# Kernel tuning notes

Hardware: AMD Instinct MI355X
Metric: run time of the kernel (lower is better)

Reference implementation:

```python
import jax, jax.numpy as jnp
import numpy as np

DIM = 2048
NUM_HEADS = 16
HEAD_DIM = DIM // NUM_HEADS
SCALE = 1.0 / float(np.sqrt(HEAD_DIM))


def setup_inputs() -> dict:
    key = jax.random.key(0)
    ks = jax.random.split(key, 7)
    B, L = 2, 2048
    x = jax.random.normal(ks[0], (B, L, DIM), dtype=jnp.float32)
    s = 1.0 / np.sqrt(DIM)
    # nn.Linear stores weight as [out, in]; y = x @ W.T + b
    Wq = jax.random.uniform(ks[1], (DIM, DIM), jnp.float32, -s, s)
    bq = jax.random.uniform(ks[2], (DIM,), jnp.float32, -s, s)
    Wk = jax.random.uniform(ks[3], (DIM, DIM), jnp.float32, -s, s)
    bk = jax.random.uniform(ks[4], (DIM,), jnp.float32, -s, s)
    Wv = jax.random.uniform(ks[5], (DIM, DIM), jnp.float32, -s, s)
    bv = jax.random.uniform(ks[6], (DIM,), jnp.float32, -s, s)
    return {"x": x, "Wq": Wq, "bq": bq, "Wk": Wk, "bk": bk, "Wv": Wv, "bv": bv}


def _attn(x, Wq, bq, Wk, bk, Wv, bv):
    B, L, D = x.shape
    H, Hd = NUM_HEADS, HEAD_DIM
    # projections: x @ W.T + b, then split heads -> [B, H, L, Hd]
    q = (x @ Wq.T + bq).reshape(B, L, H, Hd).transpose(0, 2, 1, 3)
    k = (x @ Wk.T + bk).reshape(B, L, H, Hd).transpose(0, 2, 1, 3)
    v = (x @ Wv.T + bv).reshape(B, L, H, Hd).transpose(0, 2, 1, 3)
    scores = jnp.einsum("bhqd,bhkd->bhqk", q, k) * SCALE  # [B,H,L,L]
    attn = jax.nn.softmax(scores, axis=-1)
    out = jnp.einsum("bhqk,bhkd->bhqd", attn, v)
    return out.transpose(0, 2, 1, 3).reshape(B, L, D)


def reference(x, Wq, bq, Wk, bk, Wv, bv):
    return _attn(x, Wq, bq, Wk, bk, Wv, bv)
```

## Files before the change

### kernel.cpp

```cpp
#include <hip/hip_runtime.h>
#include <stdint.h>

typedef unsigned short u16;
typedef __attribute__((ext_vector_type(8))) short short8;
typedef __attribute__((ext_vector_type(16))) float f32x16;

#define ATTN_SCALE 0.08838834764831845f

__device__ __forceinline__ u16 f2bf(float f) {
  union { float f; uint32_t u; } a; a.f = f;
  return (u16)((a.u + 0x7fffu + ((a.u >> 16) & 1u)) >> 16);
}

__device__ __forceinline__ void async16(const u16* g, u16* lds) {
  __builtin_amdgcn_global_load_lds(
      (const __attribute__((address_space(1))) void*)g,
      (__attribute__((address_space(3))) void*)lds, 16, 0, 0);
}

__global__ void cvt_kernel(const float* __restrict__ src, u16* __restrict__ dst, int n8) {
  int i = blockIdx.x * 256 + threadIdx.x;
  if (i >= n8) return;
  const float4* s4 = (const float4*)src;
  float4 a = s4[2 * i], c = s4[2 * i + 1];
  union { u16 h[8]; uint4 v; } o;
  o.h[0] = f2bf(a.x); o.h[1] = f2bf(a.y); o.h[2] = f2bf(a.z); o.h[3] = f2bf(a.w);
  o.h[4] = f2bf(c.x); o.h[5] = f2bf(c.y); o.h[6] = f2bf(c.z); o.h[7] = f2bf(c.w);
  ((uint4*)dst)[i] = o.v;
}

__global__ void cvtw_kernel(const float* __restrict__ w0, const float* __restrict__ w1,
                            const float* __restrict__ w2, u16* __restrict__ dst) {
  int z = blockIdx.y;
  const float* src = (z == 0) ? w0 : (z == 1) ? w1 : w2;
  int i = blockIdx.x * 256 + threadIdx.x;
  const float4* s4 = (const float4*)src;
  float4 a = s4[2 * i], c = s4[2 * i + 1];
  union { u16 h[8]; uint4 v; } o;
  o.h[0] = f2bf(a.x); o.h[1] = f2bf(a.y); o.h[2] = f2bf(a.z); o.h[3] = f2bf(a.w);
  o.h[4] = f2bf(c.x); o.h[5] = f2bf(c.y); o.h[6] = f2bf(c.z); o.h[7] = f2bf(c.w);
  ((uint4*)(dst + (size_t)z * 4194304))[i] = o.v;
}

__global__ __launch_bounds__(256, 4) void qkv_gemm(
    const u16* __restrict__ xb, const u16* __restrict__ Wb,
    const float* __restrict__ bq, const float* __restrict__ bk, const float* __restrict__ bv,
    u16* __restrict__ qkv) {
  __shared__ __align__(16) u16 As[2][128 * 32];
  __shared__ __align__(16) u16 Bs[2][128 * 32];
  const int z = blockIdx.z;
  const int n0 = blockIdx.x * 128, m0 = blockIdx.y * 128;
  const u16* Bw = Wb + (size_t)z * (2048u * 2048u);
  const float* bias = (z == 0) ? bq : (z == 1) ? bk : bv;
  u16* dst = qkv + (size_t)z * 8388608u;
  const int t = threadIdx.x, wave = t >> 6, lane = t & 63;
  const int wm = wave >> 1, wn = wave & 1, l31 = lane & 31, h = lane >> 5;

  int soff[2], goff[2];
#pragma unroll
  for (int p = 0; p < 2; ++p) {
    const int s = p * 256 + wave * 64 + lane;
    const int R = s >> 4, j = s & 15, u = j ^ (R & 15);
    const int m = R * 4 + (u >> 2), c = u & 3;
    soff[p] = s * 8;
    goff[p] = m * 2048 + c * 8;
  }
  int fr16[2][2], fR15[2][2];
  const int q4 = (l31 & 3) * 4;
#pragma unroll
  for (int i = 0; i < 2; ++i) {
    const int mA = wm * 64 + i * 32 + l31, mB = wn * 64 + i * 32 + l31;
    fr16[0][i] = (mA >> 2) * 16; fR15[0][i] = (mA >> 2) & 15;
    fr16[1][i] = (mB >> 2) * 16; fR15[1][i] = (mB >> 2) & 15;
  }

  f32x16 acc[2][2];
#pragma unroll
  for (int i = 0; i < 2; ++i)
#pragma unroll
    for (int j = 0; j < 2; ++j)
#pragma unroll
      for (int r = 0; r < 16; ++r) acc[i][j][r] = 0.f;

  const u16* Abase = xb + (size_t)m0 * 2048;
  const u16* Bbase = Bw + (size_t)n0 * 2048;

#pragma unroll 1
  for (int n = 0; n < 64; ++n) {
    if (n == 0) {
#pragma unroll
      for (int p = 0; p < 2; ++p) {
        async16(Abase + goff[p], &As[0][soff[p]]);
        async16(Bbase + goff[p], &Bs[0][soff[p]]);
      }
    }
    __syncthreads();
    const int cur = n & 1;
    if (n + 1 < 64) {
      const int k1 = (n + 1) * 32;
#pragma unroll
      for (int p = 0; p < 2; ++p) {
        async16(Abase + goff[p] + k1, &As[cur ^ 1][soff[p]]);
        async16(Bbase + goff[p] + k1, &Bs[cur ^ 1][soff[p]]);
      }
    }
#pragma unroll
    for (int ks = 0; ks < 2; ++ks) {
      const int c = ks * 2 + h;
      short8 af[2], bf[2];
#pragma unroll
      for (int i = 0; i < 2; ++i) {
        af[i] = *(const short8*)&As[cur][(fr16[0][i] + ((q4 + c) ^ fR15[0][i])) * 8];
        bf[i] = *(const short8*)&Bs[cur][(fr16[1][i] + ((q4 + c) ^ fR15[1][i])) * 8];
      }
#pragma unroll
      for (int i = 0; i < 2; ++i)
#pragma unroll
        for (int j = 0; j < 2; ++j)
          acc[i][j] = __builtin_amdgcn_mfma_f32_32x32x16_bf16(af[i], bf[j], acc[i][j], 0, 0, 0);
    }
  }

#pragma unroll
  for (int j = 0; j < 2; ++j) {
    const int col = n0 + wn * 64 + j * 32 + l31;
    const float bb_ = bias[col];
    const int hh = col >> 7, hd = col & 127;
#pragma unroll
    for (int i = 0; i < 2; ++i) {
#pragma unroll
      for (int g = 0; g < 4; ++g) {
        const int lbase = m0 + wm * 64 + i * 32 + 8 * g + 4 * h;
        const int bb = lbase >> 11, l0 = lbase & 2047;
        if (z == 2) {
          union { u16 q[4]; uint2 d; } pk;
#pragma unroll
          for (int rr = 0; rr < 4; ++rr) pk.q[rr] = f2bf(acc[i][j][4 * g + rr] + bb_);
          *(uint2*)&dst[((size_t)(bb * 16 + hh) * 128 + hd) * 2048 + l0] = pk.d;
        } else {
#pragma unroll
          for (int rr = 0; rr < 4; ++rr)
            dst[((size_t)(bb * 16 + hh) * 2048 + (l0 + rr)) * 128 + hd] =
                f2bf(acc[i][j][4 * g + rr] + bb_);
        }
      }
    }
  }
}

__global__ __launch_bounds__(256, 1) void attn_kernel(
    const u16* __restrict__ Qg,
    const u16* __restrict__ Kg,
    const u16* __restrict__ Vtg,
    float* __restrict__ out) {
  __shared__ __align__(16) u16 Ks[2][64 * 128];
  __shared__ __align__(16) u16 Vs[2][128 * 64];
  const int bh = blockIdx.y, q0 = blockIdx.x * 256;
  const int t = threadIdx.x, wave = t >> 6, lane = t & 63;
  const int l31 = lane & 31, h = lane >> 5;
  const u16* Qp = Qg + (size_t)bh * 262144;
  const u16* Kp = Kg + (size_t)bh * 262144;
  const u16* Vp = Vtg + (size_t)bh * 262144;
  const int b = bh >> 4, hd = bh & 15;

  short8 qf[2][8];
#pragma unroll
  for (int qs = 0; qs < 2; ++qs) {
    const int qrow = q0 + wave * 64 + qs * 32 + l31;
#pragma unroll
    for (int s = 0; s < 8; ++s)
      qf[qs][s] = *(const short8*)&Qp[(size_t)qrow * 128 + s * 16 + h * 8];
  }

  int kOff[4], kSlot[4], vOff[4], vSlot[4];
#pragma unroll
  for (int p = 0; p < 4; ++p) {
    const int s = p * 256 + wave * 64 + lane;
    const int rk = s >> 4, gk = (s & 15) ^ (rk & 15);
    kSlot[p] = s * 8; kOff[p] = rk * 128 + gk * 8;
    const int rv = s >> 3, gv = (s & 7) ^ (rv & 7);
    vSlot[p] = s * 8; vOff[p] = rv * 2048 + gv * 8;
  }

  f32x16 oac[2][4];
#pragma unroll
  for (int qs = 0; qs < 2; ++qs)
#pragma unroll
    for (int dt = 0; dt < 4; ++dt)
#pragma unroll
      for (int r = 0; r < 16; ++r) oac[qs][dt][r] = 0.f;
  float den[2] = {0.f, 0.f};

#pragma unroll 1
  for (int n = 0; n < 32; ++n) {
    if (n == 0) {
#pragma unroll
      for (int p = 0; p < 4; ++p) {
        async16(Kp + kOff[p], &Ks[0][kSlot[p]]);
        async16(Vp + vOff[p], &Vs[0][vSlot[p]]);
      }
    }
    __syncthreads();
    const int cur = n & 1;
    if (n + 1 < 32) {
      const int k1 = (n + 1) * 64;
#pragma unroll
      for (int p = 0; p < 4; ++p) {
        async16(Kp + (size_t)k1 * 128 + kOff[p], &Ks[cur ^ 1][kSlot[p]]);
        async16(Vp + (size_t)k1 + vOff[p], &Vs[cur ^ 1][vSlot[p]]);
      }
    }

#pragma unroll
    for (int T = 0; T < 2; ++T) {
      const int krow = T * 32 + l31;
      f32x16 sc[2];
#pragma unroll
      for (int qs = 0; qs < 2; ++qs)
#pragma unroll
        for (int r = 0; r < 16; ++r) sc[qs][r] = 0.f;
#pragma unroll
      for (int s = 0; s < 8; ++s) {
        const short8 kf = *(const short8*)&Ks[cur][(krow * 16 + ((2 * s + h) ^ (krow & 15))) * 8];
        sc[0] = __builtin_amdgcn_mfma_f32_32x32x16_bf16(kf, qf[0][s], sc[0], 0, 0, 0);
        sc[1] = __builtin_amdgcn_mfma_f32_32x32x16_bf16(kf, qf[1][s], sc[1], 0, 0, 0);
      }
      uint32_t pp[2][8], x[2][8];
#pragma unroll
      for (int qs = 0; qs < 2; ++qs) {
#pragma unroll
        for (int i = 0; i < 8; ++i) {
          const float e0 = __expf(fminf(sc[qs][2 * i] * ATTN_SCALE, 80.f));
          const float e1 = __expf(fminf(sc[qs][2 * i + 1] * ATTN_SCALE, 80.f));
          den[qs] += e0 + e1;
          union { float f; uint32_t u; } u0, u1; u0.f = e0; u1.f = e1;
          pp[qs][i] = ((u1.u + 0x8000u) & 0xffff0000u) | ((u0.u + 0x8000u) >> 16);
        }
#pragma unroll
        for (int i = 0; i < 8; ++i) x[qs][i] = __shfl_xor(pp[qs][i], 32, 64);
      }
#pragma unroll
      for (int ks = 0; ks < 2; ++ks) {
        const int o0 = ks * 4;
        union { uint32_t u[4]; short8 s8; } bfp[2];
#pragma unroll
        for (int qs = 0; qs < 2; ++qs) {
          bfp[qs].u[0] = h ? x[qs][o0 + 2] : pp[qs][o0 + 0];
          bfp[qs].u[1] = h ? x[qs][o0 + 3] : pp[qs][o0 + 1];
          bfp[qs].u[2] = h ? pp[qs][o0 + 2] : x[qs][o0 + 0];
          bfp[qs].u[3] = h ? pp[qs][o0 + 3] : x[qs][o0 + 1];
        }
        const int gk = T * 4 + ks * 2 + h;
#pragma unroll
        for (int dt = 0; dt < 4; ++dt) {
          const int vrow = dt * 32 + l31;
          const short8 vf = *(const short8*)&Vs[cur][(vrow * 8 + (gk ^ (vrow & 7))) * 8];
          oac[0][dt] = __builtin_amdgcn_mfma_f32_32x32x16_bf16(vf, bfp[0].s8, oac[0][dt], 0, 0, 0);
          oac[1][dt] = __builtin_amdgcn_mfma_f32_32x32x16_bf16(vf, bfp[1].s8, oac[1][dt], 0, 0, 0);
        }
      }
    }
  }

#pragma unroll
  for (int qs = 0; qs < 2; ++qs) {
    float d2 = den[qs] + __shfl_xor(den[qs], 32, 64);
    const float inv = 1.f / d2;
    const int qrow = q0 + wave * 64 + qs * 32 + l31;
#pragma unroll
    for (int dt = 0; dt < 4; ++dt) {
#pragma unroll
      for (int g4 = 0; g4 < 4; ++g4) {
        float4 o;
        o.x = oac[qs][dt][4 * g4 + 0] * inv;
        o.y = oac[qs][dt][4 * g4 + 1] * inv;
        o.z = oac[qs][dt][4 * g4 + 2] * inv;
        o.w = oac[qs][dt][4 * g4 + 3] * inv;
        const int d = dt * 32 + g4 * 8 + h * 4;
        *(float4*)&out[((size_t)(b * 2048 + qrow)) * 2048 + hd * 128 + d] = o;
      }
    }
  }
}

extern "C" void kernel_launch(void* const* d_in, const int* in_sizes, int n_in,
                              void* d_out, int out_size, void* d_ws, size_t ws_size,
                              hipStream_t stream) {
  const float* x  = (const float*)d_in[0];
  const float* Wq = (const float*)d_in[1];
  const float* bq = (const float*)d_in[2];
  const float* Wk = (const float*)d_in[3];
  const float* bk = (const float*)d_in[4];
  const float* Wv = (const float*)d_in[5];
  const float* bv = (const float*)d_in[6];
  float* out = (float*)d_out;
  if (ws_size < 92274688u) return;

  u16* xb  = (u16*)d_ws;
  u16* Wb  = xb + 8388608;
  u16* qkv = Wb + 12582912;

  cvt_kernel<<<4096, 256, 0, stream>>>(x, xb, 1048576);
  cvtw_kernel<<<dim3(2048, 3), 256, 0, stream>>>(Wq, Wk, Wv, Wb);
  qkv_gemm<<<dim3(16, 32, 3), 256, 0, stream>>>(xb, Wb, bq, bk, bv, qkv);
  attn_kernel<<<dim3(8, 32), 256, 0, stream>>>(qkv, qkv + 8388608, qkv + 16777216, out);
}
```

Before: 384.7 us.

## Split attention key tiles across wave pairs and reduce partial outputs in LDS

Each attention block now covers 128 queries instead of 256. Its four waves form two query groups times two key-half groups: each wave handles one 32-key sub-tile per 64-key chunk and keeps its own output accumulator. The partial outputs and denominators are combined through an LDS union that reuses the K/V buffers, and the launch bound allows two blocks per CU. The goal is to double the grid from 256 to 512 blocks so the 256 CUs are better filled and latency is hidden. The cost is halved K/V reuse per block, extra LDS reduction traffic and syncs, and more register pressure under the 2-block bound.

After: 391.2 us. Within noise of the previous version (+1.7%).

```diff
diff --git a/kernel.cpp b/kernel.cpp
--- a/kernel.cpp
+++ b/kernel.cpp
@@ -148,16 +148,19 @@
   }
 }
 
-__global__ __launch_bounds__(256, 1) void attn_kernel(
+__global__ __launch_bounds__(256, 2) void attn_kernel(
     const u16* __restrict__ Qg,
     const u16* __restrict__ Kg,
     const u16* __restrict__ Vtg,
     float* __restrict__ out) {
-  __shared__ __align__(16) u16 Ks[2][64 * 128];
-  __shared__ __align__(16) u16 Vs[2][128 * 64];
-  const int bh = blockIdx.y, q0 = blockIdx.x * 256;
+  __shared__ __align__(16) union {
+    struct { u16 Ks[2][64 * 128]; u16 Vs[2][128 * 64]; } lp;
+    struct { float dred[2][128]; float Ored[2][64][136]; } ep;
+  } sm;
+  const int bh = blockIdx.y, q0 = blockIdx.x * 128;
   const int t = threadIdx.x, wave = t >> 6, lane = t & 63;
   const int l31 = lane & 31, h = lane >> 5;
+  const int qg = wave & 1, T = wave >> 1;
   const u16* Qp = Qg + (size_t)bh * 262144;
   const u16* Kp = Kg + (size_t)bh * 262144;
   const u16* Vp = Vtg + (size_t)bh * 262144;
@@ -166,21 +169,22 @@
   short8 qf[2][8];
 #pragma unroll
   for (int qs = 0; qs < 2; ++qs) {
-    const int qrow = q0 + wave * 64 + qs * 32 + l31;
+    const int qrow = q0 + qg * 64 + qs * 32 + l31;
 #pragma unroll
     for (int s = 0; s < 8; ++s)
       qf[qs][s] = *(const short8*)&Qp[(size_t)qrow * 128 + s * 16 + h * 8];
   }
 
-  int kOff[4], kSlot[4], vOff[4], vSlot[4];
+  int kOff[4], vOff[4];
 #pragma unroll
   for (int p = 0; p < 4; ++p) {
     const int s = p * 256 + wave * 64 + lane;
     const int rk = s >> 4, gk = (s & 15) ^ (rk & 15);
-    kSlot[p] = s * 8; kOff[p] = rk * 128 + gk * 8;
+    kOff[p] = rk * 128 + gk * 8;
     const int rv = s >> 3, gv = (s & 7) ^ (rv & 7);
-    vSlot[p] = s * 8; vOff[p] = rv * 2048 + gv * 8;
-  }
+    vOff[p] = rv * 2048 + gv * 8;
+  }
+  const int slot0 = (wave * 64 + lane) * 8;
 
   f32x16 oac[2][4];
 #pragma unroll
@@ -190,14 +194,15 @@
 #pragma unroll
       for (int r = 0; r < 16; ++r) oac[qs][dt][r] = 0.f;
   float den[2] = {0.f, 0.f};
+  const int krow = T * 32 + l31;
 
 #pragma unroll 1
   for (int n = 0; n < 32; ++n) {
     if (n == 0) {
 #pragma unroll
       for (int p = 0; p < 4; ++p) {
-        async16(Kp + kOff[p], &Ks[0][kSlot[p]]);
-        async16(Vp + vOff[p], &Vs[0][vSlot[p]]);
+        async16(Kp + kOff[p], &sm.lp.Ks[0][slot0 + p * 2048]);
+        async16(Vp + vOff[p], &sm.lp.Vs[0][slot0 + p * 2048]);
       }
     }
     __syncthreads();
@@ -206,79 +211,100 @@
       const int k1 = (n + 1) * 64;
 #pragma unroll
       for (int p = 0; p < 4; ++p) {
-        async16(Kp + (size_t)k1 * 128 + kOff[p], &Ks[cur ^ 1][kSlot[p]]);
-        async16(Vp + (size_t)k1 + vOff[p], &Vs[cur ^ 1][vSlot[p]]);
-      }
-    }
-
-#pragma unroll
-    for (int T = 0; T < 2; ++T) {
-      const int krow = T * 32 + l31;
-      f32x16 sc[2];
-#pragma unroll
-      for (int qs = 0; qs < 2; ++qs)
-#pragma unroll
-        for (int r = 0; r < 16; ++r) sc[qs][r] = 0.f;
-#pragma unroll
-      for (int s = 0; s < 8; ++s) {
-        const short8 kf = *(const short8*)&Ks[cur][(krow * 16 + ((2 * s + h) ^ (krow & 15))) * 8];
-        sc[0] = __builtin_amdgcn_mfma_f32_32x32x16_bf16(kf, qf[0][s], sc[0], 0, 0, 0);
-        sc[1] = __builtin_amdgcn_mfma_f32_32x32x16_bf16(kf, qf[1][s], sc[1], 0, 0, 0);
-      }
-      uint32_t pp[2][8], x[2][8];
+        async16(Kp + (size_t)k1 * 128 + kOff[p], &sm.lp.Ks[cur ^ 1][slot0 + p * 2048]);
+        async16(Vp + (size_t)k1 + vOff[p], &sm.lp.Vs[cur ^ 1][slot0 + p * 2048]);
+      }
+    }
+
+    f32x16 sc[2];
+#pragma unroll
+    for (int qs = 0; qs < 2; ++qs)
+#pragma unroll
+      for (int r = 0; r < 16; ++r) sc[qs][r] = 0.f;
+#pragma unroll
+    for (int s = 0; s < 8; ++s) {
+      const short8 kf = *(const short8*)&sm.lp.Ks[cur][(krow * 16 + ((2 * s + h) ^ (krow & 15))) * 8];
+      sc[0] = __builtin_amdgcn_mfma_f32_32x32x16_bf16(kf, qf[0][s], sc[0], 0, 0, 0);
+      sc[1] = __builtin_amdgcn_mfma_f32_32x32x16_bf16(kf, qf[1][s], sc[1], 0, 0, 0);
+    }
+    uint32_t pp[2][8];
+#pragma unroll
+    for (int qs = 0; qs < 2; ++qs) {
+#pragma unroll
+      for (int i = 0; i < 8; ++i) {
+        const float e0 = __expf(fminf(sc[qs][2 * i] * ATTN_SCALE, 80.f));
+        const float e1 = __expf(fminf(sc[qs][2 * i + 1] * ATTN_SCALE, 80.f));
+        den[qs] += e0 + e1;
+        union { float f; uint32_t u; } u0, u1; u0.f = e0; u1.f = e1;
+        pp[qs][i] = ((u1.u + 0x8000u) & 0xffff0000u) | ((u0.u + 0x8000u) >> 16);
+      }
+    }
+#pragma unroll
+    for (int ks = 0; ks < 2; ++ks) {
+      const int o0 = ks * 4;
+      union { uint32_t u[4]; short8 s8; } bfp[2];
 #pragma unroll
       for (int qs = 0; qs < 2; ++qs) {
-#pragma unroll
-        for (int i = 0; i < 8; ++i) {
-          const float e0 = __expf(fminf(sc[qs][2 * i] * ATTN_SCALE, 80.f));
-          const float e1 = __expf(fminf(sc[qs][2 * i + 1] * ATTN_SCALE, 80.f));
-          den[qs] += e0 + e1;
-          union { float f; uint32_t u; } u0, u1; u0.f = e0; u1.f = e1;
-          pp[qs][i] = ((u1.u + 0x8000u) & 0xffff0000u) | ((u0.u + 0x8000u) >> 16);
+        const uint32_t x0 = __shfl_xor(pp[qs][o0 + 0], 32, 64);
+        const uint32_t x1 = __shfl_xor(pp[qs][o0 + 1], 32, 64);
+        const uint32_t x2 = __shfl_xor(pp[qs][o0 + 2], 32, 64);
+        const uint32_t x3 = __shfl_xor(pp[qs][o0 + 3], 32, 64);
+        bfp[qs].u[0] = h ? x2 : pp[qs][o0 + 0];
+        bfp[qs].u[1] = h ? x3 : pp[qs][o0 + 1];
+        bfp[qs].u[2] = h ? pp[qs][o0 + 2] : x0;
+        bfp[qs].u[3] = h ? pp[qs][o0 + 3] : x1;
+      }
+      const int gk = T * 4 + ks * 2 + h;
+#pragma unroll
+      for (int dt = 0; dt < 4; ++dt) {
+        const int vrow = dt * 32 + l31;
+        const short8 vf = *(const short8*)&sm.lp.Vs[cur][(vrow * 8 + (gk ^ (vrow & 7))) * 8];
+        oac[0][dt] = __builtin_amdgcn_mfma_f32_32x32x16_bf16(vf, bfp[0].s8, oac[0][dt], 0, 0, 0);
+        oac[1][dt] = __builtin_amdgcn_mfma_f32_32x32x16_bf16(vf, bfp[1].s8, oac[1][dt], 0, 0, 0);
+      }
+    }
+  }
+
+  den[0] += __shfl_xor(den[0], 32, 64);
+  den[1] += __shfl_xor(den[1], 32, 64);
+  __syncthreads();
+  if (h == 0) {
+    sm.ep.dred[T][qg * 64 + l31]      = den[0];
+    sm.ep.dred[T][qg * 64 + 32 + l31] = den[1];
+  }
+  if (T == 0) {
+#pragma unroll
+    for (int qs = 0; qs < 2; ++qs)
+#pragma unroll
+      for (int dt = 0; dt < 4; ++dt)
+#pragma unroll
+        for (int g = 0; g < 4; ++g) {
+          float4 w;
+          w.x = oac[qs][dt][4 * g + 0]; w.y = oac[qs][dt][4 * g + 1];
+          w.z = oac[qs][dt][4 * g + 2]; w.w = oac[qs][dt][4 * g + 3];
+          *(float4*)&sm.ep.Ored[qg][qs * 32 + l31][dt * 32 + 8 * g + 4 * h] = w;
         }
-#pragma unroll
-        for (int i = 0; i < 8; ++i) x[qs][i] = __shfl_xor(pp[qs][i], 32, 64);
-      }
-#pragma unroll
-      for (int ks = 0; ks < 2; ++ks) {
-        const int o0 = ks * 4;
-        union { uint32_t u[4]; short8 s8; } bfp[2];
-#pragma unroll
-        for (int qs = 0; qs < 2; ++qs) {
-          bfp[qs].u[0] = h ? x[qs][o0 + 2] : pp[qs][o0 + 0];
-          bfp[qs].u[1] = h ? x[qs][o0 + 3] : pp[qs][o0 + 1];
-          bfp[qs].u[2] = h ? pp[qs][o0 + 2] : x[qs][o0 + 0];
-          bfp[qs].u[3] = h ? pp[qs][o0 + 3] : x[qs][o0 + 1];
+  }
+  __syncthreads();
+  if (T == 1) {
+#pragma unroll
+    for (int qs = 0; qs < 2; ++qs) {
+      const int ql = qg * 64 + qs * 32 + l31;
+      const float inv = 1.f / (sm.ep.dred[0][ql] + sm.ep.dred[1][ql]);
+      const int qrow = q0 + ql;
+#pragma unroll
+      for (int dt = 0; dt < 4; ++dt)
+#pragma unroll
+        for (int g = 0; g < 4; ++g) {
+          const int d0 = dt * 32 + 8 * g + 4 * h;
+          const float4 v = *(const float4*)&sm.ep.Ored[qg][qs * 32 + l31][d0];
+          float4 o;
+          o.x = (v.x + oac[qs][dt][4 * g + 0]) * inv;
+          o.y = (v.y + oac[qs][dt][4 * g + 1]) * inv;
+          o.z = (v.z + oac[qs][dt][4 * g + 2]) * inv;
+          o.w = (v.w + oac[qs][dt][4 * g + 3]) * inv;
+          *(float4*)&out[((size_t)(b * 2048 + qrow)) * 2048 + hd * 128 + d0] = o;
         }
-        const int gk = T * 4 + ks * 2 + h;
-#pragma unroll
-        for (int dt = 0; dt < 4; ++dt) {
-          const int vrow = dt * 32 + l31;
-          const short8 vf = *(const short8*)&Vs[cur][(vrow * 8 + (gk ^ (vrow & 7))) * 8];
-          oac[0][dt] = __builtin_amdgcn_mfma_f32_32x32x16_bf16(vf, bfp[0].s8, oac[0][dt], 0, 0, 0);
-          oac[1][dt] = __builtin_amdgcn_mfma_f32_32x32x16_bf16(vf, bfp[1].s8, oac[1][dt], 0, 0, 0);
-        }
-      }
-    }
-  }
-
-#pragma unroll
-  for (int qs = 0; qs < 2; ++qs) {
-    float d2 = den[qs] + __shfl_xor(den[qs], 32, 64);
-    const float inv = 1.f / d2;
-    const int qrow = q0 + wave * 64 + qs * 32 + l31;
-#pragma unroll
-    for (int dt = 0; dt < 4; ++dt) {
-#pragma unroll
-      for (int g4 = 0; g4 < 4; ++g4) {
-        float4 o;
-        o.x = oac[qs][dt][4 * g4 + 0] * inv;
-        o.y = oac[qs][dt][4 * g4 + 1] * inv;
-        o.z = oac[qs][dt][4 * g4 + 2] * inv;
-        o.w = oac[qs][dt][4 * g4 + 3] * inv;
-        const int d = dt * 32 + g4 * 8 + h * 4;
-        *(float4*)&out[((size_t)(b * 2048 + qrow)) * 2048 + hd * 128 + d] = o;
-      }
     }
   }
 }
@@ -303,5 +329,5 @@
   cvt_kernel<<<4096, 256, 0, stream>>>(x, xb, 1048576);
   cvtw_kernel<<<dim3(2048, 3), 256, 0, stream>>>(Wq, Wk, Wv, Wb);
   qkv_gemm<<<dim3(16, 32, 3), 256, 0, stream>>>(xb, Wb, bq, bk, bv, qkv);
-  attn_kernel<<<dim3(8, 32), 256, 0, stream>>>(qkv, qkv + 8388608, qkv + 16777216, out);
-}
+  attn_kernel<<<dim3(16, 32), 256, 0, stream>>>(qkv, qkv + 8388608, qkv + 16777216, out);
+}
```
